# Performance work log

Hardware: AMD Instinct MI355X
Metric: run time of the kernel (lower is better)

## Reference

```python
import jax, jax.numpy as jnp
import numpy as np

B, C, E = 2, 128, 60000

def conv1(x, W, b):
    # pointwise conv1d: x [B,Cin,E], W [Cout,Cin], b [Cout] -> [B,Cout,E]
    return jnp.einsum('oc,bce->boe', W, x) + b[None, :, None]

def mesh_conv(x, gi, W, b):
    # MeshCNN GeMM conv: x [B,C,E], gi [B,E,4] neighbor edge ids, W [Cout,Cin,5], b [Cout]
    f = jax.vmap(lambda xb, ib: xb[:, ib])(x, gi)  # [B,C,E,4] neighbor gather
    f1, f2, f3, f4 = f[..., 0], f[..., 1], f[..., 2], f[..., 3]
    # symmetric features: [e, a+c, b+d, |a-c|, |b-d|]
    G = jnp.stack([x, f1 + f3, f2 + f4, jnp.abs(f1 - f3), jnp.abs(f2 - f4)], axis=-1)  # [B,C,E,5]
    return jnp.einsum('bces,ocs->boe', G, W) + b[None, :, None]


def setup_inputs() -> dict:
    key = jax.random.key(0)
    ks = jax.random.split(key, 16)
    s = 0.05
    return {
        'x_0': jax.random.normal(ks[0], (B, C, E), jnp.float32),
        'x_1': jax.random.normal(ks[1], (B, C, E), jnp.float32),
        'gemm': jax.random.randint(ks[2], (B, E, 4), 0, E, jnp.int32),
        'Wa_local': jax.random.normal(ks[3], (C, C), jnp.float32) * s,
        'ba_local': jax.random.normal(ks[4], (C,), jnp.float32) * s,
        'Wb_local': jax.random.normal(ks[5], (C, C), jnp.float32) * s,
        'bb_local': jax.random.normal(ks[6], (C,), jnp.float32) * s,
        'Wa_tri': jax.random.normal(ks[7], (C, C, 5), jnp.float32) * s,
        'ba_tri': jax.random.normal(ks[8], (C,), jnp.float32) * s,
        'Wb_tri': jax.random.normal(ks[9], (C, C, 5), jnp.float32) * s,
        'bb_tri': jax.random.normal(ks[10], (C,), jnp.float32) * s,
        'Wa_fuse': jax.random.normal(ks[11], (3, 2 * C), jnp.float32) * s,
        'ba_fuse': jax.random.normal(ks[12], (3,), jnp.float32) * s,
        'Wb_fuse': jax.random.normal(ks[13], (3, 2 * C), jnp.float32) * s,
        'bb_fuse': jax.random.normal(ks[14], (3,), jnp.float32) * s,
    }


def reference(x_0, x_1, gemm, Wa_local, ba_local, Wb_local, bb_local,
              Wa_tri, ba_tri, Wb_tri, bb_tri,
              Wa_fuse, ba_fuse, Wb_fuse, bb_fuse):
    a_local = conv1(x_0, Wa_local, ba_local)              # [B,C,E]
    a_tri = mesh_conv(x_0, gemm, Wa_tri, ba_tri)          # [B,C,E]
    x_a_two = jnp.concatenate([a_local, a_tri], axis=1)   # [B,2C,E]
    b_local = conv1(x_1, Wb_local, bb_local)
    b_tri = mesh_conv(x_1, gemm, Wb_tri, bb_tri)
    x_b_two = jnp.concatenate([b_local, b_tri], axis=1)
    x_a_w = conv1(x_a_two, Wa_fuse, ba_fuse)[:, None]     # [B,1,3,E]
    x_b_w = conv1(x_b_two, Wb_fuse, bb_fuse)[:, None]     # [B,1,3,E]
    return x_a_w + x_b_w
```

## Files before the change

### kernel.cpp

```cpp
#include <hip/hip_runtime.h>
#include <hip/hip_bf16.h>
#include <cstdint>

#define B_ 2
#define C_ 128
#define E_ 60000

typedef unsigned int uint32_;
typedef unsigned short ushort_;
typedef float v2f __attribute__((ext_vector_type(2)));

__device__ __forceinline__ v2f bp2(uint32_ v) {
    v2f r;
    r.x = __uint_as_float(v << 16);
    r.y = __uint_as_float(v & 0xffff0000u);
    return r;
}

__device__ __forceinline__ v2f vabs2(v2f a) {
    v2f r; r.x = fabsf(a.x); r.y = fabsf(a.y); return r;
}

__device__ __forceinline__ ushort_ f2b(float f) {
    union { float f; uint32_ u; } x; x.f = f;
    uint32_ u = x.u + 0x7fffu + ((x.u >> 16) & 1u);
    return (ushort_)(u >> 16);
}

__device__ __forceinline__ uint32_ packb(float lo, float hi) {
    return (uint32_)f2b(lo) | ((uint32_)f2b(hi) << 16);
}

__device__ __forceinline__ float swz_add(float v, const int pat) {
    switch (pat) {
    case 1:  return v + __int_as_float(__builtin_amdgcn_ds_swizzle(__float_as_int(v), 0x041F));
    case 2:  return v + __int_as_float(__builtin_amdgcn_ds_swizzle(__float_as_int(v), 0x081F));
    case 4:  return v + __int_as_float(__builtin_amdgcn_ds_swizzle(__float_as_int(v), 0x101F));
    case 8:  return v + __int_as_float(__builtin_amdgcn_ds_swizzle(__float_as_int(v), 0x201F));
    default: return v + __int_as_float(__builtin_amdgcn_ds_swizzle(__float_as_int(v), 0x401F));
    }
}

__global__ __launch_bounds__(256) void fuse_weights_kernel(
    const float* __restrict__ Wa_local, const float* __restrict__ ba_local,
    const float* __restrict__ Wb_local, const float* __restrict__ bb_local,
    const float* __restrict__ Wa_tri,  const float* __restrict__ ba_tri,
    const float* __restrict__ Wb_tri,  const float* __restrict__ bb_tri,
    const float* __restrict__ Wa_fuse, const float* __restrict__ ba_fuse,
    const float* __restrict__ Wb_fuse, const float* __restrict__ bb_fuse,
    float* __restrict__ Vw, float* __restrict__ cst)
{
    const int lane = threadIdx.x & 63;
    if (blockIdx.x < 15) {
        const int wid   = blockIdx.x * 4 + (threadIdx.x >> 6);
        const int pj    = wid / 10;
        const int chunk = wid % 10;
        const int p = pj / 3, j = pj % 3;
        const int f = chunk * 64 + lane;
        const float* Wf = p ? Wb_fuse : Wa_fuse;
        const float* Wt = p ? Wb_tri  : Wa_tri;
        const float* Wl = p ? Wb_local : Wa_local;
        float a0 = 0.f, a1 = 0.f, a2 = 0.f, a3 = 0.f;
        for (int o = 0; o < C_; o += 4) {
            a0 += Wf[j * 256 + 128 + o]     * Wt[(o)     * 640 + f];
            a1 += Wf[j * 256 + 128 + o + 1] * Wt[(o + 1) * 640 + f];
            a2 += Wf[j * 256 + 128 + o + 2] * Wt[(o + 2) * 640 + f];
            a3 += Wf[j * 256 + 128 + o + 3] * Wt[(o + 3) * 640 + f];
        }
        float acc = (a0 + a1) + (a2 + a3);
        const int s = f % 5, c = f / 5;
        if (s == 0) {
            float b0 = 0.f, b1 = 0.f, b2 = 0.f, b3 = 0.f;
            for (int o = 0; o < C_; o += 4) {
                b0 += Wf[j * 256 + o]     * Wl[(o)     * C_ + c];
                b1 += Wf[j * 256 + o + 1] * Wl[(o + 1) * C_ + c];
                b2 += Wf[j * 256 + o + 2] * Wl[(o + 2) * C_ + c];
                b3 += Wf[j * 256 + o + 3] * Wl[(o + 3) * C_ + c];
            }
            acc += (b0 + b1) + (b2 + b3);
        }
        Vw[(pj * 5 + s) * C_ + c] = acc;
    } else {
        if (threadIdx.x < 3) {
            int j = threadIdx.x;
            float acc = ba_fuse[j] + bb_fuse[j];
            for (int o = 0; o < C_; ++o) {
                acc += Wa_fuse[j * 256 + o]       * ba_local[o]
                     + Wa_fuse[j * 256 + 128 + o] * ba_tri[o]
                     + Wb_fuse[j * 256 + o]       * bb_local[o]
                     + Wb_fuse[j * 256 + 128 + o] * bb_tri[o];
            }
            cst[j] = acc;
        }
    }
}

__global__ __launch_bounds__(256) void transpose_interleave_kernel(
    const float* __restrict__ x0, const float* __restrict__ x1,
    uint32_* __restrict__ y)
{
    __shared__ float tA[32][65];
    __shared__ float tB[32][65];
    const int b  = blockIdx.z;
    const int e0 = blockIdx.x * 32;
    const int c0 = blockIdx.y * 64;
    const float* s0 = x0 + (size_t)b * C_ * E_;
    const float* s1 = x1 + (size_t)b * C_ * E_;
    const int t = threadIdx.x;
    {
        const int c  = t >> 2;
        const int e8 = (t & 3) * 8;
        const float* p0 = s0 + (size_t)(c0 + c) * E_ + e0 + e8;
        const float* p1 = s1 + (size_t)(c0 + c) * E_ + e0 + e8;
        float4 u0 = *(const float4*)p0;
        float4 u1 = *(const float4*)(p0 + 4);
        float4 v0 = *(const float4*)p1;
        float4 v1 = *(const float4*)(p1 + 4);
        tA[e8 + 0][c] = u0.x; tA[e8 + 1][c] = u0.y;
        tA[e8 + 2][c] = u0.z; tA[e8 + 3][c] = u0.w;
        tA[e8 + 4][c] = u1.x; tA[e8 + 5][c] = u1.y;
        tA[e8 + 6][c] = u1.z; tA[e8 + 7][c] = u1.w;
        tB[e8 + 0][c] = v0.x; tB[e8 + 1][c] = v0.y;
        tB[e8 + 2][c] = v0.z; tB[e8 + 3][c] = v0.w;
        tB[e8 + 4][c] = v1.x; tB[e8 + 5][c] = v1.y;
        tB[e8 + 6][c] = v1.z; tB[e8 + 7][c] = v1.w;
    }
    __syncthreads();
    {
        const int e  = t >> 3;
        const int c8 = (t & 7) * 8;
        const float* ra = &tA[e][c8];
        const float* rb = &tB[e][c8];
        uint4 w0, w1;
        w0.x = packb(ra[0], ra[1]); w0.y = packb(rb[0], rb[1]);
        w0.z = packb(ra[2], ra[3]); w0.w = packb(rb[2], rb[3]);
        w1.x = packb(ra[4], ra[5]); w1.y = packb(rb[4], rb[5]);
        w1.z = packb(ra[6], ra[7]); w1.w = packb(rb[6], rb[7]);
        uint32_* drow = y + (((size_t)(b * E_ + e0 + e)) << 7) + c0 + c8;
        *(uint4*)(drow)     = w0;
        *(uint4*)(drow + 4) = w1;
    }
}

__global__ __launch_bounds__(256, 4) void mesh_fused_kernel(
    const uint2* __restrict__ y, const int* __restrict__ gemm,
    const float* __restrict__ Vw, const float* __restrict__ cst,
    float* __restrict__ out)
{
    const int lane = threadIdx.x & 63;
    const int wv   = threadIdx.x >> 6;
    const int gw   = blockIdx.x * 4 + wv;
    const int nw   = gridDim.x * 4;

    v2f w[2][3][5];
#pragma unroll
    for (int p = 0; p < 2; ++p)
#pragma unroll
        for (int j = 0; j < 3; ++j)
#pragma unroll
            for (int s = 0; s < 5; ++s)
                w[p][j][s] = *(const v2f*)(Vw + (((p * 3 + j) * 5 + s) << 7) + lane * 2);

    const int  jj     = lane >> 4;
    const bool is0    = (jj == 0), is1 = (jj == 1);
    const bool writer = ((lane & 15) == 0) && (jj < 3);
    const float cj    = is0 ? cst[0] : (is1 ? cst[1] : cst[2]);
    float* obase      = out + (size_t)(jj < 3 ? jj : 2) * E_;

    const int4* g4 = (const int4*)gemm;
    const int npair = (B_ * E_) / 2;

    int4 giA = make_int4(0, 0, 0, 0), giB = giA;
    if (gw < npair) { giA = g4[2 * gw]; giB = g4[2 * gw + 1]; }

    for (int pair = gw; pair < npair; pair += nw) {
        const int nxt = pair + nw;
        const int4 gA = giA, gB = giB;
        if (nxt < npair) { giA = g4[2 * nxt]; giB = g4[2 * nxt + 1]; }

        const int e0 = 2 * pair;
        const int b  = (e0 >= E_) ? 1 : 0;
        const int e  = e0 - (b ? E_ : 0);
        const uint2* Y = y + (size_t)b * (E_ * 64);

        const uint32_ sA  = ((uint32_)e    << 6) + lane;
        const uint32_ sB  = sA + 64;
        const uint32_ oA1 = ((uint32_)gA.x << 6) + lane;
        const uint32_ oA2 = ((uint32_)gA.y << 6) + lane;
        const uint32_ oA3 = ((uint32_)gA.z << 6) + lane;
        const uint32_ oA4 = ((uint32_)gA.w << 6) + lane;
        const uint32_ oB1 = ((uint32_)gB.x << 6) + lane;
        const uint32_ oB2 = ((uint32_)gB.y << 6) + lane;
        const uint32_ oB3 = ((uint32_)gB.z << 6) + lane;
        const uint32_ oB4 = ((uint32_)gB.w << 6) + lane;

        const uint2 PA0 = Y[sA],  PA1 = Y[oA1], PA2 = Y[oA2],
                    PA3 = Y[oA3], PA4 = Y[oA4];
        const uint2 PB0 = Y[sB],  PB1 = Y[oB1], PB2 = Y[oB2],
                    PB3 = Y[oB3], PB4 = Y[oB4];

        float rA0, rA1, rA2;
        {
            v2f a0 = bp2(PA0.x), a1 = bp2(PA1.x), a2 = bp2(PA2.x),
                a3 = bp2(PA3.x), a4 = bp2(PA4.x);
            v2f b0 = bp2(PA0.y), b1 = bp2(PA1.y), b2 = bp2(PA2.y),
                b3 = bp2(PA3.y), b4 = bp2(PA4.y);
            v2f sa1 = a1 + a3, sa2 = a2 + a4;
            v2f da1 = vabs2(a1 - a3), da2 = vabs2(a2 - a4);
            v2f sb1 = b1 + b3, sb2 = b2 + b4;
            v2f db1 = vabs2(b1 - b3), db2 = vabs2(b2 - b4);
            v2f t0 = w[0][0][0] * a0, t1 = w[0][1][0] * a0, t2 = w[0][2][0] * a0;
            t0 += w[0][0][1] * sa1; t1 += w[0][1][1] * sa1; t2 += w[0][2][1] * sa1;
            t0 += w[0][0][2] * sa2; t1 += w[0][1][2] * sa2; t2 += w[0][2][2] * sa2;
            t0 += w[0][0][3] * da1; t1 += w[0][1][3] * da1; t2 += w[0][2][3] * da1;
            t0 += w[0][0][4] * da2; t1 += w[0][1][4] * da2; t2 += w[0][2][4] * da2;
            t0 += w[1][0][0] * b0;  t1 += w[1][1][0] * b0;  t2 += w[1][2][0] * b0;
            t0 += w[1][0][1] * sb1; t1 += w[1][1][1] * sb1; t2 += w[1][2][1] * sb1;
            t0 += w[1][0][2] * sb2; t1 += w[1][1][2] * sb2; t2 += w[1][2][2] * sb2;
            t0 += w[1][0][3] * db1; t1 += w[1][1][3] * db1; t2 += w[1][2][3] * db1;
            t0 += w[1][0][4] * db2; t1 += w[1][1][4] * db2; t2 += w[1][2][4] * db2;
            rA0 = t0.x + t0.y; rA1 = t1.x + t1.y; rA2 = t2.x + t2.y;
        }
        float rB0, rB1, rB2;
        {
            v2f a0 = bp2(PB0.x), a1 = bp2(PB1.x), a2 = bp2(PB2.x),
                a3 = bp2(PB3.x), a4 = bp2(PB4.x);
            v2f b0 = bp2(PB0.y), b1 = bp2(PB1.y), b2 = bp2(PB2.y),
                b3 = bp2(PB3.y), b4 = bp2(PB4.y);
            v2f sa1 = a1 + a3, sa2 = a2 + a4;
            v2f da1 = vabs2(a1 - a3), da2 = vabs2(a2 - a4);
            v2f sb1 = b1 + b3, sb2 = b2 + b4;
            v2f db1 = vabs2(b1 - b3), db2 = vabs2(b2 - b4);
            v2f t0 = w[0][0][0] * a0, t1 = w[0][1][0] * a0, t2 = w[0][2][0] * a0;
            t0 += w[0][0][1] * sa1; t1 += w[0][1][1] * sa1; t2 += w[0][2][1] * sa1;
            t0 += w[0][0][2] * sa2; t1 += w[0][1][2] * sa2; t2 += w[0][2][2] * sa2;
            t0 += w[0][0][3] * da1; t1 += w[0][1][3] * da1; t2 += w[0][2][3] * da1;
            t0 += w[0][0][4] * da2; t1 += w[0][1][4] * da2; t2 += w[0][2][4] * da2;
            t0 += w[1][0][0] * b0;  t1 += w[1][1][0] * b0;  t2 += w[1][2][0] * b0;
            t0 += w[1][0][1] * sb1; t1 += w[1][1][1] * sb1; t2 += w[1][2][1] * sb1;
            t0 += w[1][0][2] * sb2; t1 += w[1][1][2] * sb2; t2 += w[1][2][2] * sb2;
            t0 += w[1][0][3] * db1; t1 += w[1][1][3] * db1; t2 += w[1][2][3] * db1;
            t0 += w[1][0][4] * db2; t1 += w[1][1][4] * db2; t2 += w[1][2][4] * db2;
            rB0 = t0.x + t0.y; rB1 = t1.x + t1.y; rB2 = t2.x + t2.y;
        }

        rA0 = swz_add(rA0, 16); rB0 = swz_add(rB0, 16);
        rA1 = swz_add(rA1, 16); rB1 = swz_add(rB1, 16);
        rA2 = swz_add(rA2, 16); rB2 = swz_add(rB2, 16);
        rA0 += __shfl_xor(rA0, 32, 64); rB0 += __shfl_xor(rB0, 32, 64);
        rA1 += __shfl_xor(rA1, 32, 64); rB1 += __shfl_xor(rB1, 32, 64);
        rA2 += __shfl_xor(rA2, 32, 64); rB2 += __shfl_xor(rB2, 32, 64);

        float vA = is0 ? rA0 : (is1 ? rA1 : rA2);
        float vB = is0 ? rB0 : (is1 ? rB1 : rB2);
        vA = swz_add(vA, 1); vB = swz_add(vB, 1);
        vA = swz_add(vA, 2); vB = swz_add(vB, 2);
        vA = swz_add(vA, 4); vB = swz_add(vB, 4);
        vA = swz_add(vA, 8); vB = swz_add(vB, 8);

        if (writer) {
            float2 st; st.x = vA + cj; st.y = vB + cj;
            *(float2*)(obase + (b ? 3 * E_ : 0) + e) = st;
        }
    }
}

extern "C" void kernel_launch(void* const* d_in, const int* in_sizes, int n_in,
                              void* d_out, int out_size, void* d_ws, size_t ws_size,
                              hipStream_t stream) {
    const float* x0       = (const float*)d_in[0];
    const float* x1       = (const float*)d_in[1];
    const int*   gemm     = (const int*)d_in[2];
    const float* Wa_local = (const float*)d_in[3];
    const float* ba_local = (const float*)d_in[4];
    const float* Wb_local = (const float*)d_in[5];
    const float* bb_local = (const float*)d_in[6];
    const float* Wa_tri   = (const float*)d_in[7];
    const float* ba_tri   = (const float*)d_in[8];
    const float* Wb_tri   = (const float*)d_in[9];
    const float* bb_tri   = (const float*)d_in[10];
    const float* Wa_fuse  = (const float*)d_in[11];
    const float* ba_fuse  = (const float*)d_in[12];
    const float* Wb_fuse  = (const float*)d_in[13];
    const float* bb_fuse  = (const float*)d_in[14];
    float* out = (float*)d_out;

    uint32_* y   = (uint32_*)d_ws;
    float*   Vw  = (float*)(y + (size_t)B_ * E_ * 128);
    float*   cst = Vw + 2 * 3 * 5 * C_;

    hipLaunchKernelGGL(fuse_weights_kernel, dim3(16), dim3(256), 0, stream,
                       Wa_local, ba_local, Wb_local, bb_local,
                       Wa_tri, ba_tri, Wb_tri, bb_tri,
                       Wa_fuse, ba_fuse, Wb_fuse, bb_fuse, Vw, cst);

    hipLaunchKernelGGL(transpose_interleave_kernel, dim3(E_ / 32, C_ / 64, B_),
                       dim3(256), 0, stream, x0, x1, y);

    hipLaunchKernelGGL(mesh_fused_kernel, dim3(2048), dim3(256), 0, stream,
                       (const uint2*)y, gemm, Vw, cst, out);
}
```

Measured before the change: 227.7 us.

## Double-buffer neighbor gathers in mesh kernel and widen transpose tiles

The mesh kernel now uses two register buffers and a ping-pong loop, so the gathers for the next edge pair are issued before the current pair is computed and stored. This hides gather latency in exchange for more registers, and occupancy is lowered from 4 to 3 blocks per CU to fit them. The transpose kernel now processes 64 edges per block instead of 32, with clamped loads and a bounds check on the ragged tail. Weights move from an array to named scalars.

```diff
diff --git a/kernel.cpp b/kernel.cpp
--- a/kernel.cpp
+++ b/kernel.cpp
@@ -99,51 +99,119 @@
     const float* __restrict__ x0, const float* __restrict__ x1,
     uint32_* __restrict__ y)
 {
-    __shared__ float tA[32][65];
-    __shared__ float tB[32][65];
+    __shared__ float tA[64][65];
+    __shared__ float tB[64][65];
     const int b  = blockIdx.z;
-    const int e0 = blockIdx.x * 32;
+    const int e0 = blockIdx.x * 64;
     const int c0 = blockIdx.y * 64;
-    const float* s0 = x0 + (size_t)b * C_ * E_;
-    const float* s1 = x1 + (size_t)b * C_ * E_;
+    const float* s0 = x0 + (size_t)b * C_ * E_ + (size_t)c0 * E_;
+    const float* s1 = x1 + (size_t)b * C_ * E_ + (size_t)c0 * E_;
     const int t = threadIdx.x;
     {
-        const int c  = t >> 2;
-        const int e8 = (t & 3) * 8;
-        const float* p0 = s0 + (size_t)(c0 + c) * E_ + e0 + e8;
-        const float* p1 = s1 + (size_t)(c0 + c) * E_ + e0 + e8;
-        float4 u0 = *(const float4*)p0;
-        float4 u1 = *(const float4*)(p0 + 4);
-        float4 v0 = *(const float4*)p1;
-        float4 v1 = *(const float4*)(p1 + 4);
-        tA[e8 + 0][c] = u0.x; tA[e8 + 1][c] = u0.y;
-        tA[e8 + 2][c] = u0.z; tA[e8 + 3][c] = u0.w;
-        tA[e8 + 4][c] = u1.x; tA[e8 + 5][c] = u1.y;
-        tA[e8 + 6][c] = u1.z; tA[e8 + 7][c] = u1.w;
-        tB[e8 + 0][c] = v0.x; tB[e8 + 1][c] = v0.y;
-        tB[e8 + 2][c] = v0.z; tB[e8 + 3][c] = v0.w;
-        tB[e8 + 4][c] = v1.x; tB[e8 + 5][c] = v1.y;
-        tB[e8 + 6][c] = v1.z; tB[e8 + 7][c] = v1.w;
+        const int c   = t >> 2;
+        const int e16 = (t & 3) * 16;
+        const float* p0 = s0 + (size_t)c * E_;
+        const float* p1 = s1 + (size_t)c * E_;
+#pragma unroll
+        for (int i = 0; i < 4; ++i) {
+            int ea = e0 + e16 + 4 * i;
+            ea = (ea > E_ - 4) ? (E_ - 4) : ea;
+            float4 u = *(const float4*)(p0 + ea);
+            float4 v = *(const float4*)(p1 + ea);
+            const int el = e16 + 4 * i;
+            tA[el + 0][c] = u.x; tA[el + 1][c] = u.y;
+            tA[el + 2][c] = u.z; tA[el + 3][c] = u.w;
+            tB[el + 0][c] = v.x; tB[el + 1][c] = v.y;
+            tB[el + 2][c] = v.z; tB[el + 3][c] = v.w;
+        }
     }
     __syncthreads();
     {
-        const int e  = t >> 3;
-        const int c8 = (t & 7) * 8;
-        const float* ra = &tA[e][c8];
-        const float* rb = &tB[e][c8];
-        uint4 w0, w1;
-        w0.x = packb(ra[0], ra[1]); w0.y = packb(rb[0], rb[1]);
-        w0.z = packb(ra[2], ra[3]); w0.w = packb(rb[2], rb[3]);
-        w1.x = packb(ra[4], ra[5]); w1.y = packb(rb[4], rb[5]);
-        w1.z = packb(ra[6], ra[7]); w1.w = packb(rb[6], rb[7]);
-        uint32_* drow = y + (((size_t)(b * E_ + e0 + e)) << 7) + c0 + c8;
-        *(uint4*)(drow)     = w0;
-        *(uint4*)(drow + 4) = w1;
-    }
-}
-
-__global__ __launch_bounds__(256, 4) void mesh_fused_kernel(
-    const uint2* __restrict__ y, const int* __restrict__ gemm,
+        const int e   = t >> 2;
+        const int k16 = (t & 3) * 16;
+        const int er  = e0 + e;
+        if (er < E_) {
+            const float* ra = &tA[e][k16];
+            const float* rb = &tB[e][k16];
+            uint32_* drow = y + (((size_t)(b * E_ + er)) << 7) + c0 + k16;
+#pragma unroll
+            for (int m = 0; m < 4; ++m) {
+                uint4 w_;
+                w_.x = packb(ra[4 * m],     ra[4 * m + 1]);
+                w_.y = packb(rb[4 * m],     rb[4 * m + 1]);
+                w_.z = packb(ra[4 * m + 2], ra[4 * m + 3]);
+                w_.w = packb(rb[4 * m + 2], rb[4 * m + 3]);
+                *(uint4*)(drow + 4 * m) = w_;
+            }
+        }
+    }
+}
+
+#define LDW(p, j, s) (*(const v2f*)(Vw + ((((p) * 3 + (j)) * 5 + (s)) << 7) + (lane << 1)))
+
+#define ISSUE(B0,B1,B2,B3,B4,B5,B6,B7,B8,B9, gA, gB, pr) do {                 \
+    const int ee0_ = 2 * (pr);                                                \
+    const int bb_  = (ee0_ >= E_) ? 1 : 0;                                    \
+    const int ee_  = ee0_ - (bb_ ? E_ : 0);                                   \
+    const uint2* Yb_ = yy + (size_t)bb_ * (E_ * 64);                          \
+    const uint32_ s0_ = ((uint32_)ee_ << 6) + lane;                           \
+    B1 = Yb_[((uint32_)(gA).x << 6) + lane];                                  \
+    B2 = Yb_[((uint32_)(gA).y << 6) + lane];                                  \
+    B3 = Yb_[((uint32_)(gA).z << 6) + lane];                                  \
+    B4 = Yb_[((uint32_)(gA).w << 6) + lane];                                  \
+    B6 = Yb_[((uint32_)(gB).x << 6) + lane];                                  \
+    B7 = Yb_[((uint32_)(gB).y << 6) + lane];                                  \
+    B8 = Yb_[((uint32_)(gB).z << 6) + lane];                                  \
+    B9 = Yb_[((uint32_)(gB).w << 6) + lane];                                  \
+    B0 = Yb_[s0_];                                                            \
+    B5 = Yb_[s0_ + 64];                                                       \
+} while (0)
+
+#define EDGE_DOT(P0,P1,P2,P3,P4, R0,R1,R2) do {                               \
+    v2f a0 = bp2(P0.x), a1 = bp2(P1.x), a2 = bp2(P2.x),                       \
+        a3 = bp2(P3.x), a4 = bp2(P4.x);                                       \
+    v2f b0 = bp2(P0.y), b1 = bp2(P1.y), b2 = bp2(P2.y),                       \
+        b3 = bp2(P3.y), b4 = bp2(P4.y);                                       \
+    v2f sa1 = a1 + a3, sa2 = a2 + a4;                                         \
+    v2f da1 = vabs2(a1 - a3), da2 = vabs2(a2 - a4);                           \
+    v2f sb1 = b1 + b3, sb2 = b2 + b4;                                         \
+    v2f db1 = vabs2(b1 - b3), db2 = vabs2(b2 - b4);                           \
+    v2f t0 = w000 * a0 + w001 * sa1 + w002 * sa2 + w003 * da1 + w004 * da2    \
+           + w100 * b0 + w101 * sb1 + w102 * sb2 + w103 * db1 + w104 * db2;   \
+    v2f t1 = w010 * a0 + w011 * sa1 + w012 * sa2 + w013 * da1 + w014 * da2    \
+           + w110 * b0 + w111 * sb1 + w112 * sb2 + w113 * db1 + w114 * db2;   \
+    v2f t2 = w020 * a0 + w021 * sa1 + w022 * sa2 + w023 * da1 + w024 * da2    \
+           + w120 * b0 + w121 * sb1 + w122 * sb2 + w123 * db1 + w124 * db2;   \
+    R0 = t0.x + t0.y; R1 = t1.x + t1.y; R2 = t2.x + t2.y;                     \
+} while (0)
+
+#define COMPSTORE(B0,B1,B2,B3,B4,B5,B6,B7,B8,B9, pr) do {                     \
+    float rA0, rA1, rA2, rB0, rB1, rB2;                                       \
+    EDGE_DOT(B0, B1, B2, B3, B4, rA0, rA1, rA2);                              \
+    EDGE_DOT(B5, B6, B7, B8, B9, rB0, rB1, rB2);                              \
+    rA0 = swz_add(rA0, 16); rB0 = swz_add(rB0, 16);                           \
+    rA1 = swz_add(rA1, 16); rB1 = swz_add(rB1, 16);                           \
+    rA2 = swz_add(rA2, 16); rB2 = swz_add(rB2, 16);                           \
+    rA0 += __shfl_xor(rA0, 32, 64); rB0 += __shfl_xor(rB0, 32, 64);           \
+    rA1 += __shfl_xor(rA1, 32, 64); rB1 += __shfl_xor(rB1, 32, 64);           \
+    rA2 += __shfl_xor(rA2, 32, 64); rB2 += __shfl_xor(rB2, 32, 64);           \
+    float vA = is0 ? rA0 : (is1 ? rA1 : rA2);                                 \
+    float vB = is0 ? rB0 : (is1 ? rB1 : rB2);                                 \
+    vA = swz_add(vA, 1); vB = swz_add(vB, 1);                                 \
+    vA = swz_add(vA, 2); vB = swz_add(vB, 2);                                 \
+    vA = swz_add(vA, 4); vB = swz_add(vB, 4);                                 \
+    vA = swz_add(vA, 8); vB = swz_add(vB, 8);                                 \
+    if (writer) {                                                             \
+        const int ee0_ = 2 * (pr);                                            \
+        const int bb_  = (ee0_ >= E_) ? 1 : 0;                                \
+        const int ee_  = ee0_ - (bb_ ? E_ : 0);                               \
+        float2 st; st.x = vA + cj; st.y = vB + cj;                            \
+        *(float2*)(obase + (bb_ ? 3 * E_ : 0) + ee_) = st;                    \
+    }                                                                         \
+} while (0)
+
+__global__ __launch_bounds__(256, 3) void mesh_fused_kernel(
+    const uint2* __restrict__ yy, const int* __restrict__ gemm,
     const float* __restrict__ Vw, const float* __restrict__ cst,
     float* __restrict__ out)
 {
@@ -152,14 +220,18 @@
     const int gw   = blockIdx.x * 4 + wv;
     const int nw   = gridDim.x * 4;
 
-    v2f w[2][3][5];
-#pragma unroll
-    for (int p = 0; p < 2; ++p)
-#pragma unroll
-        for (int j = 0; j < 3; ++j)
-#pragma unroll
-            for (int s = 0; s < 5; ++s)
-                w[p][j][s] = *(const v2f*)(Vw + (((p * 3 + j) * 5 + s) << 7) + lane * 2);
+    v2f w000 = LDW(0,0,0), w001 = LDW(0,0,1), w002 = LDW(0,0,2),
+        w003 = LDW(0,0,3), w004 = LDW(0,0,4);
+    v2f w010 = LDW(0,1,0), w011 = LDW(0,1,1), w012 = LDW(0,1,2),
+        w013 = LDW(0,1,3), w014 = LDW(0,1,4);
+    v2f w020 = LDW(0,2,0), w021 = LDW(0,2,1), w022 = LDW(0,2,2),
+        w023 = LDW(0,2,3), w024 = LDW(0,2,4);
+    v2f w100 = LDW(1,0,0), w101 = LDW(1,0,1), w102 = LDW(1,0,2),
+        w103 = LDW(1,0,3), w104 = LDW(1,0,4);
+    v2f w110 = LDW(1,1,0), w111 = LDW(1,1,1), w112 = LDW(1,1,2),
+        w113 = LDW(1,1,3), w114 = LDW(1,1,4);
+    v2f w120 = LDW(1,2,0), w121 = LDW(1,2,1), w122 = LDW(1,2,2),
+        w123 = LDW(1,2,3), w124 = LDW(1,2,4);
 
     const int  jj     = lane >> 4;
     const bool is0    = (jj == 0), is1 = (jj == 1);
@@ -170,97 +242,33 @@
     const int4* g4 = (const int4*)gemm;
     const int npair = (B_ * E_) / 2;
 
-    int4 giA = make_int4(0, 0, 0, 0), giB = giA;
-    if (gw < npair) { giA = g4[2 * gw]; giB = g4[2 * gw + 1]; }
-
-    for (int pair = gw; pair < npair; pair += nw) {
-        const int nxt = pair + nw;
-        const int4 gA = giA, gB = giB;
-        if (nxt < npair) { giA = g4[2 * nxt]; giB = g4[2 * nxt + 1]; }
-
-        const int e0 = 2 * pair;
-        const int b  = (e0 >= E_) ? 1 : 0;
-        const int e  = e0 - (b ? E_ : 0);
-        const uint2* Y = y + (size_t)b * (E_ * 64);
-
-        const uint32_ sA  = ((uint32_)e    << 6) + lane;
-        const uint32_ sB  = sA + 64;
-        const uint32_ oA1 = ((uint32_)gA.x << 6) + lane;
-        const uint32_ oA2 = ((uint32_)gA.y << 6) + lane;
-        const uint32_ oA3 = ((uint32_)gA.z << 6) + lane;
-        const uint32_ oA4 = ((uint32_)gA.w << 6) + lane;
-        const uint32_ oB1 = ((uint32_)gB.x << 6) + lane;
-        const uint32_ oB2 = ((uint32_)gB.y << 6) + lane;
-        const uint32_ oB3 = ((uint32_)gB.z << 6) + lane;
-        const uint32_ oB4 = ((uint32_)gB.w << 6) + lane;
-
-        const uint2 PA0 = Y[sA],  PA1 = Y[oA1], PA2 = Y[oA2],
-                    PA3 = Y[oA3], PA4 = Y[oA4];
-        const uint2 PB0 = Y[sB],  PB1 = Y[oB1], PB2 = Y[oB2],
-                    PB3 = Y[oB3], PB4 = Y[oB4];
-
-        float rA0, rA1, rA2;
+    int pc = gw;
+    if (pc >= npair) return;
+
+    uint2 A0, A1, A2, A3, A4, A5, A6, A7, A8, A9;
+    uint2 D0, D1, D2, D3, D4, D5, D6, D7, D8, D9;
+
+    int4 giA = g4[2 * pc], giB = g4[2 * pc + 1];
+    ISSUE(A0,A1,A2,A3,A4,A5,A6,A7,A8,A9, giA, giB, pc);
+    int pn = pc + nw;
+    if (pn < npair) { giA = g4[2 * pn]; giB = g4[2 * pn + 1]; }
+
+    for (;;) {
+        if (pn >= npair) { COMPSTORE(A0,A1,A2,A3,A4,A5,A6,A7,A8,A9, pc); break; }
+        ISSUE(D0,D1,D2,D3,D4,D5,D6,D7,D8,D9, giA, giB, pn);
         {
-            v2f a0 = bp2(PA0.x), a1 = bp2(PA1.x), a2 = bp2(PA2.x),
-                a3 = bp2(PA3.x), a4 = bp2(PA4.x);
-            v2f b0 = bp2(PA0.y), b1 = bp2(PA1.y), b2 = bp2(PA2.y),
-                b3 = bp2(PA3.y), b4 = bp2(PA4.y);
-            v2f sa1 = a1 + a3, sa2 = a2 + a4;
-            v2f da1 = vabs2(a1 - a3), da2 = vabs2(a2 - a4);
-            v2f sb1 = b1 + b3, sb2 = b2 + b4;
-            v2f db1 = vabs2(b1 - b3), db2 = vabs2(b2 - b4);
-            v2f t0 = w[0][0][0] * a0, t1 = w[0][1][0] * a0, t2 = w[0][2][0] * a0;
-            t0 += w[0][0][1] * sa1; t1 += w[0][1][1] * sa1; t2 += w[0][2][1] * sa1;
-            t0 += w[0][0][2] * sa2; t1 += w[0][1][2] * sa2; t2 += w[0][2][2] * sa2;
-            t0 += w[0][0][3] * da1; t1 += w[0][1][3] * da1; t2 += w[0][2][3] * da1;
-            t0 += w[0][0][4] * da2; t1 += w[0][1][4] * da2; t2 += w[0][2][4] * da2;
-            t0 += w[1][0][0] * b0;  t1 += w[1][1][0] * b0;  t2 += w[1][2][0] * b0;
-            t0 += w[1][0][1] * sb1; t1 += w[1][1][1] * sb1; t2 += w[1][2][1] * sb1;
-            t0 += w[1][0][2] * sb2; t1 += w[1][1][2] * sb2; t2 += w[1][2][2] * sb2;
-            t0 += w[1][0][3] * db1; t1 += w[1][1][3] * db1; t2 += w[1][2][3] * db1;
-            t0 += w[1][0][4] * db2; t1 += w[1][1][4] * db2; t2 += w[1][2][4] * db2;
-            rA0 = t0.x + t0.y; rA1 = t1.x + t1.y; rA2 = t2.x + t2.y;
-        }
-        float rB0, rB1, rB2;
+            const int pf = pn + nw;
+            if (pf < npair) { giA = g4[2 * pf]; giB = g4[2 * pf + 1]; }
+            COMPSTORE(A0,A1,A2,A3,A4,A5,A6,A7,A8,A9, pc);
+            pc = pn; pn = pf;
+        }
+        if (pn >= npair) { COMPSTORE(D0,D1,D2,D3,D4,D5,D6,D7,D8,D9, pc); break; }
+        ISSUE(A0,A1,A2,A3,A4,A5,A6,A7,A8,A9, giA, giB, pn);
         {
-            v2f a0 = bp2(PB0.x), a1 = bp2(PB1.x), a2 = bp2(PB2.x),
-                a3 = bp2(PB3.x), a4 = bp2(PB4.x);
-            v2f b0 = bp2(PB0.y), b1 = bp2(PB1.y), b2 = bp2(PB2.y),
-                b3 = bp2(PB3.y), b4 = bp2(PB4.y);
-            v2f sa1 = a1 + a3, sa2 = a2 + a4;
-            v2f da1 = vabs2(a1 - a3), da2 = vabs2(a2 - a4);
-            v2f sb1 = b1 + b3, sb2 = b2 + b4;
-            v2f db1 = vabs2(b1 - b3), db2 = vabs2(b2 - b4);
-            v2f t0 = w[0][0][0] * a0, t1 = w[0][1][0] * a0, t2 = w[0][2][0] * a0;
-            t0 += w[0][0][1] * sa1; t1 += w[0][1][1] * sa1; t2 += w[0][2][1] * sa1;
-            t0 += w[0][0][2] * sa2; t1 += w[0][1][2] * sa2; t2 += w[0][2][2] * sa2;
-            t0 += w[0][0][3] * da1; t1 += w[0][1][3] * da1; t2 += w[0][2][3] * da1;
-            t0 += w[0][0][4] * da2; t1 += w[0][1][4] * da2; t2 += w[0][2][4] * da2;
-            t0 += w[1][0][0] * b0;  t1 += w[1][1][0] * b0;  t2 += w[1][2][0] * b0;
-            t0 += w[1][0][1] * sb1; t1 += w[1][1][1] * sb1; t2 += w[1][2][1] * sb1;
-            t0 += w[1][0][2] * sb2; t1 += w[1][1][2] * sb2; t2 += w[1][2][2] * sb2;
-            t0 += w[1][0][3] * db1; t1 += w[1][1][3] * db1; t2 += w[1][2][3] * db1;
-            t0 += w[1][0][4] * db2; t1 += w[1][1][4] * db2; t2 += w[1][2][4] * db2;
-            rB0 = t0.x + t0.y; rB1 = t1.x + t1.y; rB2 = t2.x + t2.y;
-        }
-
-        rA0 = swz_add(rA0, 16); rB0 = swz_add(rB0, 16);
-        rA1 = swz_add(rA1, 16); rB1 = swz_add(rB1, 16);
-        rA2 = swz_add(rA2, 16); rB2 = swz_add(rB2, 16);
-        rA0 += __shfl_xor(rA0, 32, 64); rB0 += __shfl_xor(rB0, 32, 64);
-        rA1 += __shfl_xor(rA1, 32, 64); rB1 += __shfl_xor(rB1, 32, 64);
-        rA2 += __shfl_xor(rA2, 32, 64); rB2 += __shfl_xor(rB2, 32, 64);
-
-        float vA = is0 ? rA0 : (is1 ? rA1 : rA2);
-        float vB = is0 ? rB0 : (is1 ? rB1 : rB2);
-        vA = swz_add(vA, 1); vB = swz_add(vB, 1);
-        vA = swz_add(vA, 2); vB = swz_add(vB, 2);
-        vA = swz_add(vA, 4); vB = swz_add(vB, 4);
-        vA = swz_add(vA, 8); vB = swz_add(vB, 8);
-
-        if (writer) {
-            float2 st; st.x = vA + cj; st.y = vB + cj;
-            *(float2*)(obase + (b ? 3 * E_ : 0) + e) = st;
+            const int pf = pn + nw;
+            if (pf < npair) { giA = g4[2 * pf]; giB = g4[2 * pf + 1]; }
+            COMPSTORE(D0,D1,D2,D3,D4,D5,D6,D7,D8,D9, pc);
+            pc = pn; pn = pf;
         }
     }
 }
@@ -294,7 +302,8 @@
                        Wa_tri, ba_tri, Wb_tri, bb_tri,
                        Wa_fuse, ba_fuse, Wb_fuse, bb_fuse, Vw, cst);
 
-    hipLaunchKernelGGL(transpose_interleave_kernel, dim3(E_ / 32, C_ / 64, B_),
+    hipLaunchKernelGGL(transpose_interleave_kernel,
+                       dim3((E_ + 63) / 64, C_ / 64, B_),
                        dim3(256), 0, stream, x0, x1, y);
 
     hipLaunchKernelGGL(mesh_fused_kernel, dim3(2048), dim3(256), 0, stream,
```

New measurement: 236.5 us. +3.9%, slower.
